# Performance work log

Measured on AMD Instinct MI355X. Metric: run time of the kernel, lower is better.

The kernel has to match this reference:

```python
import jax, jax.numpy as jnp
import numpy as np
from jax.scipy.special import erfc

# ---- model constants (mirroring NeuroNN.__init__ defaults) ----
NEURON_NUM = 6000
RATIO = 0.8
NE = int(NEURON_NUM * RATIO)   # excitatory count (pref ordering: E first)
NI = NEURON_NUM - NE           # inhibitory count (connection blocks: first NI rows/cols)
SCALING_G = 1.0
W_FF = 30.0
SIG_EXT = 5.0
TAU = 1.0
TAU_REF = 1.0
T_INV = 1.0
VT, VR = 20.0, 10.0            # LIF threshold / reset (mV) used inside Ricciardi Phi
DT = 0.1
NMAX = 80                      # Euler2fixedpt total steps (fixed for jit)
NAVG = 30                      # convergence-averaging window
XTOL = 1e-5
XMIN = 1.0

# 64-pt Gauss-Legendre quadrature for the Ricciardi integral
_qn, _qw = np.polynomial.legendre.leggauss(64)
QN = jnp.asarray(_qn, jnp.float32)
QW = jnp.asarray(_qw, jnp.float32)
SQRT_PI = float(np.sqrt(np.pi))


def erfcx(y):
    """Scaled complementary error function exp(y^2)*erfc(y), fp32-safe."""
    y = jnp.clip(y, -9.0, 25.0)  # exp(81) still finite in fp32
    a = jnp.abs(y)
    a_s = jnp.minimum(a, 5.0)
    small = jnp.exp(a_s * a_s) * erfc(a_s)
    a_l = jnp.maximum(a, 5.0)
    large = (1.0 / (SQRT_PI * a_l)) * (1.0 - 0.5 / (a_l * a_l))
    f = jnp.where(a <= 5.0, small, large)
    return jnp.where(y >= 0.0, f, 2.0 * jnp.exp(y * y) - f)


def circ_gauss(x_deg, w):
    # circular gaussian with period 180 deg, same form as the z-row kernel
    return jnp.exp((jnp.cos(x_deg * jnp.pi / 90.0) - 1.0) / (4.0 * (jnp.pi / 180.0 * w) ** 2))


def phi(mu, sigma, tau, tau_ref):
    """Ricciardi LIF transfer: 1/(tau_ref + tau*sqrt(pi)*int_l^u erfcx(-x) dx)."""
    u = (VT - mu) / sigma
    l = (VR - mu) / sigma
    c = 0.5 * (u + l)
    h = 0.5 * (u - l)
    x = c[:, None] + h[:, None] * QN[None, :]          # [N, 64]
    integ = h * jnp.sum(QW[None, :] * erfcx(-x), axis=1)
    return 1.0 / (tau_ref + tau * SQRT_PI * jnp.maximum(integ, 0.0))


def setup_inputs() -> dict:
    key = jax.random.key(0)
    k1, k2, k3 = jax.random.split(key, 3)
    # hyperparameters = [J; P; w], exactly the module's init values
    hyperparameters = jnp.array([[1.99, 1.9, -1.01, -0.79],
                                 [0.11, 0.11, 0.45, 0.45],
                                 [32.0, 32.0, 32.0, 32.0]], dtype=jnp.float32)
    contrast = jax.random.uniform(k1, (1,), jnp.float32)                 # [0,1)
    grating_orientations = jax.random.uniform(k2, (1,), jnp.float32) * 180.0
    # self.pref: E then I linspace over [0,180)
    pref = np.concatenate([np.linspace(0.0, 180.0, NE, endpoint=False),
                           np.linspace(0.0, 180.0, NI, endpoint=False)]).astype(np.float32)
    preferred_orientations = jnp.asarray(pref)
    rand_u = jax.random.uniform(k3, (NEURON_NUM, NEURON_NUM), jnp.float32)
    return {"hyperparameters": hyperparameters, "contrast": contrast,
            "grating_orientations": grating_orientations,
            "preferred_orientations": preferred_orientations, "rand_u": rand_u}


def reference(hyperparameters, contrast, grating_orientations, preferred_orientations, rand_u):
    N = NEURON_NUM
    eff_p, prob_p, width_p = hyperparameters[0], hyperparameters[1], hyperparameters[2]
    i = jnp.arange(N)
    ri = (i < NI).astype(jnp.int32)                      # row block (1 if row < NI)
    conn = ri[:, None] + 2 * ri[None, :]                 # 0/1/2/3 block ids [N,N]
    # circulant roll: np.roll(z_row, i)[j] = z_row[(j-i) % N]
    idx = (i[None, :] - i[:, None]) % N                  # [N,N]
    conn_rolled = ri[:, None] + 2 * (idx < NI).astype(jnp.int32)
    thetas = jnp.linspace(0.0, jnp.pi - 0.01, N)
    cos_term = (jnp.cos(2.0 * thetas) - 1.0)[idx]        # gathered, rolled per row
    width_r = width_p[conn_rolled]
    Z = jnp.exp(cos_term / (4.0 * (jnp.pi / 180.0 * width_r) ** 2))
    # W[i,j] = J * sigmoid(32*(P * z_roll - U))
    W = eff_p[conn] * jax.nn.sigmoid(32.0 * (prob_p[conn] * Z - rand_u))
    W2 = W * W
    # stimulus -> feedforward input
    input_mean = contrast * 20.0 * SCALING_G * circ_gauss(
        grating_orientations - preferred_orientations, W_FF)          # [N]
    input_sd = SIG_EXT

    def step(r, _):
        mu = TAU * (W @ r) + input_mean
        sig = jnp.sqrt(TAU * (W2 @ r) + input_sd ** 2)
        dx = T_INV * (phi(mu, sig, TAU, TAU_REF) - r) * DT
        r2 = r + dx
        conv = jnp.max(jnp.abs(dx) / jnp.maximum(XMIN, jnp.abs(r2))) < XTOL
        return r2, conv

    r0 = jnp.zeros(N, jnp.float32)
    r_fp, convs = jax.lax.scan(step, r0, None, length=NMAX)
    avg_step = jnp.mean(convs[-NAVG:].astype(jnp.float32))
    return r_fp, avg_step
```

## Files before the change

kernel.cpp:

```cpp
#include <hip/hip_runtime.h>
#include <hip/hip_fp16.h>
#include <math.h>

#define NN    6000
#define NPAD  6144
#define NIB   1200
#define NMAXI 80
#define NAVGI 30
#define NBLK  250
#define NTHR  512

#define SQRT_PI_F 1.7724538509055160273f

typedef _Float16 half2_t __attribute__((ext_vector_type(2)));
typedef unsigned uvec8  __attribute__((ext_vector_type(8)));

__device__ __forceinline__ float erfcx_inl(float y) {
  y = fminf(fmaxf(y, -9.0f), 25.0f);
  const float a   = fabsf(y);
  const float a_s = fminf(a, 5.0f);
  const float t   = 1.0f / (1.0f + 0.5f * a_s);
  const float p   = -1.26551223f + t * (1.00002368f + t * (0.37409196f +
                    t * (0.09678418f + t * (-0.18628806f + t * (0.27886807f +
                    t * (-1.13520398f + t * (1.48851587f + t * (-0.82215223f +
                    t * 0.17087277f))))))));
  const float fsm = t * __expf(p);
  const float a_l = fmaxf(a, 5.0f);
  const float flg = (1.0f / (SQRT_PI_F * a_l)) * (1.0f - 0.5f / (a_l * a_l));
  const float f   = (a <= 5.0f) ? fsm : flg;
  return (y >= 0.0f) ? f : 2.0f * __expf(y * y) - f;
}

__device__ __forceinline__ float dot2acc(unsigned w, unsigned r, float acc) {
#if defined(__has_builtin) && __has_builtin(__builtin_amdgcn_fdot2)
  return __builtin_amdgcn_fdot2(__builtin_bit_cast(half2_t, w),
                                __builtin_bit_cast(half2_t, r), acc, false);
#else
  half2_t wh = __builtin_bit_cast(half2_t, w);
  half2_t rh = __builtin_bit_cast(half2_t, r);
  return acc + (float)wh.x * (float)rh.x + (float)wh.y * (float)rh.y;
#endif
}

__device__ __forceinline__ unsigned pksq(unsigned w) {
  half2_t wh = __builtin_bit_cast(half2_t, w);
  half2_t s  = wh * wh;
  return __builtin_bit_cast(unsigned, s);
}

__device__ __forceinline__ void gbar(unsigned* cnt, unsigned* gen, int tid) {
  __syncthreads();
  if (tid == 0) {
    __builtin_amdgcn_fence(__ATOMIC_RELEASE, "agent");
    const unsigned g = __hip_atomic_load(gen, __ATOMIC_RELAXED,
                                         __HIP_MEMORY_SCOPE_AGENT);
    const unsigned old = __hip_atomic_fetch_add(cnt, 1u, __ATOMIC_RELAXED,
                                                __HIP_MEMORY_SCOPE_AGENT);
    if (old == NBLK - 1) {
      __hip_atomic_store(cnt, 0u, __ATOMIC_RELAXED, __HIP_MEMORY_SCOPE_AGENT);
      __hip_atomic_store(gen, g + 1u, __ATOMIC_RELEASE,
                         __HIP_MEMORY_SCOPE_AGENT);
    } else {
      while (__hip_atomic_load(gen, __ATOMIC_RELAXED,
                               __HIP_MEMORY_SCOPE_AGENT) == g)
        __builtin_amdgcn_s_sleep(2);
    }
    __builtin_amdgcn_fence(__ATOMIC_ACQUIRE, "agent");
  }
  __syncthreads();
}

__global__ __launch_bounds__(256) void init_kernel(
    const float* __restrict__ contrast, const float* __restrict__ grat,
    const float* __restrict__ pref, float* __restrict__ g0,
    float* __restrict__ g1, float* __restrict__ meanv,
    float* __restrict__ ctab, float* __restrict__ qn, float* __restrict__ qw,
    unsigned* __restrict__ conv, unsigned* __restrict__ bar)
{
  int t = blockIdx.x * 256 + threadIdx.x;
  if (t < NPAD) { g0[t] = 0.0f; g1[t] = 0.0f; }
  if (t < NN) {
    double th = (3.141592653589793 - 0.01) * (double)t / 5999.0;
    ctab[t] = cosf(2.0f * (float)th) - 1.0f;
    float d  = grat[0] - pref[t];
    float cg = (cosf(d * 3.14159265358979323846f / 90.0f) - 1.0f) / 1.0966227112321508f;
    meanv[t] = contrast[0] * 20.0f * expf(cg);
  }
  if (t < NMAXI) conv[t] = 0u;
  if (t < 2)     bar[t]  = 0u;
  if (blockIdx.x == 0 && threadIdx.x < 64) {
    int m = threadIdx.x;
    double x = cos(3.141592653589793 * (m + 0.75) / 64.5);
    double p0, p1, dp = 1.0;
    for (int it = 0; it < 60; ++it) {
      p0 = 1.0; p1 = x;
      for (int k = 2; k <= 64; ++k) {
        double p2 = ((2.0 * k - 1.0) * x * p1 - (k - 1.0) * p0) / (double)k;
        p0 = p1; p1 = p2;
      }
      dp = 64.0 * (x * p1 - p0) / (x * x - 1.0);
      double step = p1 / dp;
      x -= step;
      if (fabs(step) < 1e-15) break;
    }
    p0 = 1.0; p1 = x;
    for (int k = 2; k <= 64; ++k) {
      double p2 = ((2.0 * k - 1.0) * x * p1 - (k - 1.0) * p0) / (double)k;
      p0 = p1; p1 = p2;
    }
    dp = 64.0 * (x * p1 - p0) / (x * x - 1.0);
    double wgt = 2.0 / ((1.0 - x * x) * dp * dp);
    qn[63 - m] = (float)x;
    qw[63 - m] = (float)wgt;
  }
}

#define GENV(WV, ROW, V, EI, EE, PI, PE, DI, DE, UROW)                        \
  do {                                                                        \
    _Pragma("unroll")                                                         \
    for (int c_ = 0; c_ < 4; ++c_) {                                          \
      const int k_  = (V) * 4 + c_;                                           \
      const int j0_ = k_ * 256 + (lane << 2);                                 \
      float w_[4] = {0.0f, 0.0f, 0.0f, 0.0f};                                 \
      if (j0_ + 3 < NN) {                                                     \
        const float4 uv_ = *reinterpret_cast<const float4*>((UROW) + j0_);    \
        const float us_[4] = {uv_.x, uv_.y, uv_.z, uv_.w};                    \
        _Pragma("unroll")                                                     \
        for (int q_ = 0; q_ < 4; ++q_) {                                      \
          const int j_ = j0_ + q_;                                            \
          int idx_ = j_ - (ROW); idx_ += (idx_ < 0) ? NN : 0;                 \
          const float ct_   = ctabs[idx_];                                    \
          const float eff_  = (j_   < NIB) ? (EI) : (EE);                     \
          const float prob_ = (j_   < NIB) ? (PI) : (PE);                     \
          const float den_  = (idx_ < NIB) ? (DI) : (DE);                     \
          const float Z_  = __expf(ct_ / den_);                               \
          const float tt_ = 32.0f * (prob_ * Z_ - us_[q_]);                   \
          w_[q_] = eff_ / (1.0f + __expf(-tt_));                              \
        }                                                                     \
      }                                                                       \
      half2_t h01_; h01_.x = (_Float16)w_[0]; h01_.y = (_Float16)w_[1];       \
      half2_t h23_; h23_.x = (_Float16)w_[2]; h23_.y = (_Float16)w_[3];       \
      WV[2 * c_]     = __builtin_bit_cast(unsigned, h01_);                    \
      WV[2 * c_ + 1] = __builtin_bit_cast(unsigned, h23_);                    \
    }                                                                         \
  } while (0)

#define ACC3(WAV, WBV, WCV, V)                                                \
  do {                                                                        \
    _Pragma("unroll")                                                         \
    for (int c_ = 0; c_ < 4; ++c_) {                                          \
      const uint2 rr_ = rh2[((V) * 4 + c_) * 64 + lane];                      \
      muA  = dot2acc(WAV[2 * c_],       rr_.x, muA);                          \
      muA  = dot2acc(WAV[2 * c_ + 1],   rr_.y, muA);                          \
      varA = dot2acc(pksq(WAV[2 * c_]),     rr_.x, varA);                     \
      varA = dot2acc(pksq(WAV[2 * c_ + 1]), rr_.y, varA);                     \
      muB  = dot2acc(WBV[2 * c_],       rr_.x, muB);                          \
      muB  = dot2acc(WBV[2 * c_ + 1],   rr_.y, muB);                          \
      varB = dot2acc(pksq(WBV[2 * c_]),     rr_.x, varB);                     \
      varB = dot2acc(pksq(WBV[2 * c_ + 1]), rr_.y, varB);                     \
      muC  = dot2acc(WCV[2 * c_],       rr_.x, muC);                          \
      muC  = dot2acc(WCV[2 * c_ + 1],   rr_.y, muC);                          \
      varC = dot2acc(pksq(WCV[2 * c_]),     rr_.x, varC);                     \
      varC = dot2acc(pksq(WCV[2 * c_ + 1]), rr_.y, varC);                     \
    }                                                                         \
  } while (0)

__global__
__attribute__((amdgpu_flat_work_group_size(NTHR, NTHR)))
__attribute__((amdgpu_waves_per_eu(2, 2))) void solve_kernel(
    const float* __restrict__ hyper, const float* __restrict__ randu,
    const float* __restrict__ ctab, const float* __restrict__ meanv,
    const float* __restrict__ qn, const float* __restrict__ qw,
    float* __restrict__ g0, float* __restrict__ g1,
    float* __restrict__ blkmax, unsigned* __restrict__ bar,
    float* __restrict__ out)
{
  const int tid  = threadIdx.x;
  const int lane = tid & 63;
  const int wv   = tid >> 6;
  const int rowA = blockIdx.x * 24 + wv * 3;
  const int rowB = rowA + 1;
  const int rowC = rowA + 2;

  __shared__ float ctabs[NN];
  __shared__ uint2 rh2[NPAD / 4];
  __shared__ float wmax[8];
  __shared__ float sflag[NAVGI];

  {
    const float4* c4 = reinterpret_cast<const float4*>(ctab);
    float4* l4 = reinterpret_cast<float4*>(ctabs);
    for (int i = tid; i < NN / 4; i += NTHR) l4[i] = c4[i];
  }
  __syncthreads();

  const float qnl = qn[lane];
  const float qwl = qw[lane];
  const float meanA = meanv[rowA];
  const float meanB = meanv[rowB];
  const float meanC = meanv[rowC];

  uvec8 wa0, wa1, wa2, wa3, wa4, wa5;
  uvec8 wb0, wb1, wb2, wb3, wb4, wb5;
  uvec8 wc0, wc1, wc2, wc3, wc4, wc5;
  {
    const float cdg = 0.017453292519943295f;
    {
      const int   ri = (rowA < NIB) ? 1 : 0;
      const float eI = hyper[2 + ri], eE = hyper[0 + ri];
      const float pI = hyper[6 + ri], pE = hyper[4 + ri];
      const float wI = cdg * hyper[10 + ri], wE = cdg * hyper[8 + ri];
      const float dI = 4.0f * (wI * wI), dE = 4.0f * (wE * wE);
      const float* ur = randu + (size_t)rowA * NN;
      GENV(wa0, rowA, 0, eI, eE, pI, pE, dI, dE, ur);
      GENV(wa1, rowA, 1, eI, eE, pI, pE, dI, dE, ur);
      GENV(wa2, rowA, 2, eI, eE, pI, pE, dI, dE, ur);
      GENV(wa3, rowA, 3, eI, eE, pI, pE, dI, dE, ur);
      GENV(wa4, rowA, 4, eI, eE, pI, pE, dI, dE, ur);
      GENV(wa5, rowA, 5, eI, eE, pI, pE, dI, dE, ur);
    }
    {
      const int   ri = (rowB < NIB) ? 1 : 0;
      const float eI = hyper[2 + ri], eE = hyper[0 + ri];
      const float pI = hyper[6 + ri], pE = hyper[4 + ri];
      const float wI = cdg * hyper[10 + ri], wE = cdg * hyper[8 + ri];
      const float dI = 4.0f * (wI * wI), dE = 4.0f * (wE * wE);
      const float* ur = randu + (size_t)rowB * NN;
      GENV(wb0, rowB, 0, eI, eE, pI, pE, dI, dE, ur);
      GENV(wb1, rowB, 1, eI, eE, pI, pE, dI, dE, ur);
      GENV(wb2, rowB, 2, eI, eE, pI, pE, dI, dE, ur);
      GENV(wb3, rowB, 3, eI, eE, pI, pE, dI, dE, ur);
      GENV(wb4, rowB, 4, eI, eE, pI, pE, dI, dE, ur);
      GENV(wb5, rowB, 5, eI, eE, pI, pE, dI, dE, ur);
    }
    {
      const int   ri = (rowC < NIB) ? 1 : 0;
      const float eI = hyper[2 + ri], eE = hyper[0 + ri];
      const float pI = hyper[6 + ri], pE = hyper[4 + ri];
      const float wI = cdg * hyper[10 + ri], wE = cdg * hyper[8 + ri];
      const float dI = 4.0f * (wI * wI), dE = 4.0f * (wE * wE);
      const float* ur = randu + (size_t)rowC * NN;
      GENV(wc0, rowC, 0, eI, eE, pI, pE, dI, dE, ur);
      GENV(wc1, rowC, 1, eI, eE, pI, pE, dI, dE, ur);
      GENV(wc2, rowC, 2, eI, eE, pI, pE, dI, dE, ur);
      GENV(wc3, rowC, 3, eI, eE, pI, pE, dI, dE, ur);
      GENV(wc4, rowC, 4, eI, eE, pI, pE, dI, dE, ur);
      GENV(wc5, rowC, 5, eI, eE, pI, pE, dI, dE, ur);
    }
  }

#pragma unroll 1
  for (int t = 0; t < NMAXI; ++t) {
    const float* rcur = (t & 1) ? g1 : g0;
    float*       rnxt = (t & 1) ? g0 : g1;

    {
      const float4* rc4 = reinterpret_cast<const float4*>(rcur);
#pragma unroll
      for (int s = 0; s < 3; ++s) {
        const float4 s0 = rc4[tid + s * NTHR];
        half2_t a, b;
        a.x = (_Float16)s0.x; a.y = (_Float16)s0.y;
        b.x = (_Float16)s0.z; b.y = (_Float16)s0.w;
        uint2 p;
        p.x = __builtin_bit_cast(unsigned, a);
        p.y = __builtin_bit_cast(unsigned, b);
        rh2[tid + s * NTHR] = p;
      }
    }
    __syncthreads();

    float muA = 0.0f, varA = 0.0f, muB = 0.0f, varB = 0.0f;
    float muC = 0.0f, varC = 0.0f;
    ACC3(wa0, wb0, wc0, 0);
    ACC3(wa1, wb1, wc1, 1);
    ACC3(wa2, wb2, wc2, 2);
    ACC3(wa3, wb3, wc3, 3);
    ACC3(wa4, wb4, wc4, 4);
    ACC3(wa5, wb5, wc5, 5);
#pragma unroll
    for (int off = 32; off > 0; off >>= 1) {
      muA  += __shfl_xor(muA, off);
      varA += __shfl_xor(varA, off);
      muB  += __shfl_xor(muB, off);
      varB += __shfl_xor(varB, off);
      muC  += __shfl_xor(muC, off);
      varC += __shfl_xor(varC, off);
    }

    float ratioM = 0.0f;
#pragma unroll
    for (int rr = 0; rr < 3; ++rr) {
      const int   row = (rr == 0) ? rowA : (rr == 1) ? rowB : rowC;
      float mu  = ((rr == 0) ? muA  : (rr == 1) ? muB  : muC)
                + ((rr == 0) ? meanA : (rr == 1) ? meanB : meanC);
      float var = ((rr == 0) ? varA : (rr == 1) ? varB : varC) + 25.0f;
      const float sig = sqrtf(var);
      const float uu = (20.0f - mu) / sig;
      const float ll = (10.0f - mu) / sig;
      const float cc = 0.5f * (uu + ll);
      const float hh = 0.5f * (uu - ll);
      const float x = cc + hh * qnl;
      float term    = qwl * erfcx_inl(-x);
#pragma unroll
      for (int off = 32; off > 0; off >>= 1) term += __shfl_xor(term, off);
      const float integ = hh * term;
      const float phiv  = 1.0f / (1.0f + SQRT_PI_F * fmaxf(integ, 0.0f));

      const float rold = rcur[row];
      const float dx   = (phiv - rold) * 0.1f;
      const float rnew = rold + dx;
      ratioM = fmaxf(ratioM, fabsf(dx) / fmaxf(1.0f, fabsf(rnew)));
      if (lane == 0) {
        if (t == NMAXI - 1) out[row] = rnew;
        else                rnxt[row] = rnew;
      }
    }
    if (lane == 0) wmax[wv] = ratioM;
    __syncthreads();
    if (tid == 0) {
      float m = wmax[0];
#pragma unroll
      for (int q = 1; q < 8; ++q) m = fmaxf(m, wmax[q]);
      blkmax[(size_t)t * NBLK + blockIdx.x] = m;
    }
    gbar(bar, bar + 1, tid);
  }

  if (blockIdx.x == 0) {
#pragma unroll
    for (int s = 0; s < 4; ++s) {
      const int t = 50 + wv + 8 * s;
      if (t < NMAXI) {
        float m = 0.0f;
        for (int p = lane; p < NBLK; p += 64)
          m = fmaxf(m, blkmax[(size_t)t * NBLK + p]);
#pragma unroll
        for (int off = 32; off > 0; off >>= 1)
          m = fmaxf(m, __shfl_xor(m, off));
        if (lane == 0) sflag[t - 50] = (m < 1e-5f) ? 1.0f : 0.0f;
      }
    }
    __syncthreads();
    if (tid == 0) {
      float s = 0.0f;
#pragma unroll
      for (int q = 0; q < NAVGI; ++q) s += sflag[q];
      out[NN] = s / 30.0f;
    }
  }
}

__global__ __launch_bounds__(256) void genw_kernel(
    const float* __restrict__ hyper, const float* __restrict__ randu,
    const float* __restrict__ ctab, float* __restrict__ Wf)
{
  const int i  = blockIdx.x;
  const int ri = (i < NIB) ? 1 : 0;
  const float eA = hyper[0 + ri], eB = hyper[2 + ri];
  const float pA = hyper[4 + ri], pB = hyper[6 + ri];
  const float c  = 0.017453292519943295f;
  const float wA = c * hyper[8 + ri], wB = c * hyper[10 + ri];
  const float dA = 4.0f * (wA * wA), dB = 4.0f * (wB * wB);
  const float* urow = randu + (size_t)i * NN;
  for (int j4 = threadIdx.x * 4; j4 < NN; j4 += 1024) {
    float4 uv = *reinterpret_cast<const float4*>(urow + j4);
    float us[4] = {uv.x, uv.y, uv.z, uv.w};
    float res[4];
#pragma unroll
    for (int q = 0; q < 4; ++q) {
      int j   = j4 + q;
      int idx = j - i; idx += (idx < 0) ? NN : 0;
      float ct   = ctab[idx];
      float eff  = (j   < NIB) ? eB : eA;
      float prob = (j   < NIB) ? pB : pA;
      float den  = (idx < NIB) ? dB : dA;
      float Z  = __expf(ct / den);
      float tt = 32.0f * (prob * Z - us[q]);
      res[q] = eff / (1.0f + __expf(-tt));
    }
    *reinterpret_cast<float4*>(Wf + (size_t)i * NN + j4) =
        make_float4(res[0], res[1], res[2], res[3]);
  }
}

__global__ __launch_bounds__(256) void iter_kernel(
    const float* __restrict__ Wf, const float* __restrict__ rin,
    float* __restrict__ rout, const float* __restrict__ meanv,
    const float* __restrict__ qn, const float* __restrict__ qw,
    unsigned* __restrict__ convslot)
{
  const int row  = blockIdx.x;
  const int tid  = threadIdx.x;
  const int lane = tid & 63;
  const int wvid = tid >> 6;
  __shared__ float smu[4], svar[4];
  float mu = 0.0f, var = 0.0f;
  const float* wrow = Wf + (size_t)row * NN;
  float4 w[6], r4[6]; bool have[6];
#pragma unroll
  for (int k = 0; k < 6; ++k) {
    const int j = (tid << 2) + (k << 10);
    have[k] = (j < NN);
    if (have[k]) {
      w[k]  = *reinterpret_cast<const float4*>(wrow + j);
      r4[k] = *reinterpret_cast<const float4*>(rin + j);
    }
  }
#pragma unroll
  for (int k = 0; k < 6; ++k) if (have[k]) {
    mu  += w[k].x * r4[k].x + w[k].y * r4[k].y + w[k].z * r4[k].z + w[k].w * r4[k].w;
    var += w[k].x * w[k].x * r4[k].x + w[k].y * w[k].y * r4[k].y
         + w[k].z * w[k].z * r4[k].z + w[k].w * w[k].w * r4[k].w;
  }
#pragma unroll
  for (int off = 32; off > 0; off >>= 1) {
    mu  += __shfl_xor(mu, off);
    var += __shfl_xor(var, off);
  }
  if (lane == 0) { smu[wvid] = mu; svar[wvid] = var; }
  __syncthreads();
  if (tid < 64) {
    mu  = smu[0] + smu[1] + smu[2] + smu[3];
    var = svar[0] + svar[1] + svar[2] + svar[3];
    mu += meanv[row]; var += 25.0f;
    const float sig = sqrtf(var);
    const float uu = (20.0f - mu) / sig;
    const float ll = (10.0f - mu) / sig;
    const float cc = 0.5f * (uu + ll);
    const float hh = 0.5f * (uu - ll);
    const float x = cc + hh * qn[lane];
    float term    = qw[lane] * erfcx_inl(-x);
#pragma unroll
    for (int off = 32; off > 0; off >>= 1) term += __shfl_xor(term, off);
    const float integ = hh * term;
    const float phiv  = 1.0f / (1.0f + SQRT_PI_F * fmaxf(integ, 0.0f));
    const float rold = rin[row];
    const float dx   = (phiv - rold) * 0.1f;
    const float rnew = rold + dx;
    if (lane == 0) {
      rout[row] = rnew;
      const float ratio = fabsf(dx) / fmaxf(1.0f, fabsf(rnew));
      atomicMax(convslot, __float_as_uint(ratio));
    }
  }
}

__global__ __launch_bounds__(256) void final_kernel(
    const float* __restrict__ rfin, const unsigned* __restrict__ conv,
    float* __restrict__ out)
{
  int t = blockIdx.x * 256 + threadIdx.x;
  if (t < NN) out[t] = rfin[t];
  if (t == 6000) {
    float s = 0.0f;
    for (int k = NMAXI - NAVGI; k < NMAXI; ++k)
      s += (__uint_as_float(conv[k]) < 1e-5f) ? 1.0f : 0.0f;
    out[NN] = s / 30.0f;
  }
}

extern "C" void kernel_launch(void* const* d_in, const int* in_sizes, int n_in,
                              void* d_out, int out_size, void* d_ws, size_t ws_size,
                              hipStream_t stream) {
  const float* hyper    = (const float*)d_in[0];
  const float* contrast = (const float*)d_in[1];
  const float* grat     = (const float*)d_in[2];
  const float* pref     = (const float*)d_in[3];
  const float* randu    = (const float*)d_in[4];
  float* out = (float*)d_out;

  char* ws = (char*)d_ws;
  float*    g0     = (float*)(ws + 0);
  float*    g1     = (float*)(ws + 24576);
  float*    mn     = (float*)(ws + 49152);
  float*    ctab   = (float*)(ws + 73152);
  float*    qn     = (float*)(ws + 97152);
  float*    qw     = (float*)(ws + 97408);
  unsigned* conv   = (unsigned*)(ws + 97664);
  unsigned* bar    = (unsigned*)(ws + 97984);
  float*    blkmax = (float*)(ws + 98304);
  float*    Wf     = (float*)(ws + 262144);

  init_kernel<<<24, 256, 0, stream>>>(contrast, grat, pref, g0, g1, mn, ctab,
                                      qn, qw, conv, bar);

  {
    const float* a_hyper = hyper;  const float* a_randu = randu;
    const float* a_ctab  = ctab;   const float* a_mn    = mn;
    const float* a_qn    = qn;     const float* a_qw    = qw;
    float* a_g0 = g0; float* a_g1 = g1; float* a_bm = blkmax;
    unsigned* a_bar = bar; float* a_out = out;
    void* args[11] = {&a_hyper, &a_randu, &a_ctab, &a_mn, &a_qn, &a_qw,
                      &a_g0, &a_g1, &a_bm, &a_bar, &a_out};
    hipError_t err = hipLaunchCooperativeKernel(
        (const void*)solve_kernel, dim3(NBLK), dim3(NTHR), args, 0, stream);
    if (err == hipSuccess) return;
  }

  genw_kernel<<<NN, 256, 0, stream>>>(hyper, randu, ctab, Wf);
  float* rb[2] = {g0, g1};
  for (int t = 0; t < NMAXI; ++t) {
    const float* rin = rb[t & 1];
    float*       rou = rb[(t + 1) & 1];
    iter_kernel<<<NN, 256, 0, stream>>>(Wf, rin, rou, mn, qn, qw, conv + t);
  }
  final_kernel<<<24, 256, 0, stream>>>(rb[0], conv, out);
}
```

Measured before the change: 1.665 ms.

## Stream fp16 weights from global memory instead of holding them in registers

The fp16 weight rows are no longer kept resident in registers for all 80 iterations. They are written once to a global workspace buffer and re-read each iteration with 16-byte vector loads, using 8 elements per lane and a uint4 shared r-vector. This frees the very large register footprint so the waves_per_eu constraint can be dropped. In exchange, every iteration re-reads about 72 MB of weights from L2/HBM, which risks making the loop bandwidth-bound.

```diff
diff --git a/kernel.cpp b/kernel.cpp
--- a/kernel.cpp
+++ b/kernel.cpp
@@ -13,7 +13,6 @@
 #define SQRT_PI_F 1.7724538509055160273f
 
 typedef _Float16 half2_t __attribute__((ext_vector_type(2)));
-typedef unsigned uvec8  __attribute__((ext_vector_type(8)));
 
 __device__ __forceinline__ float erfcx_inl(float y) {
   y = fminf(fmaxf(y, -9.0f), 25.0f);
@@ -115,63 +114,12 @@
   }
 }
 
-#define GENV(WV, ROW, V, EI, EE, PI, PE, DI, DE, UROW)                        \
-  do {                                                                        \
-    _Pragma("unroll")                                                         \
-    for (int c_ = 0; c_ < 4; ++c_) {                                          \
-      const int k_  = (V) * 4 + c_;                                           \
-      const int j0_ = k_ * 256 + (lane << 2);                                 \
-      float w_[4] = {0.0f, 0.0f, 0.0f, 0.0f};                                 \
-      if (j0_ + 3 < NN) {                                                     \
-        const float4 uv_ = *reinterpret_cast<const float4*>((UROW) + j0_);    \
-        const float us_[4] = {uv_.x, uv_.y, uv_.z, uv_.w};                    \
-        _Pragma("unroll")                                                     \
-        for (int q_ = 0; q_ < 4; ++q_) {                                      \
-          const int j_ = j0_ + q_;                                            \
-          int idx_ = j_ - (ROW); idx_ += (idx_ < 0) ? NN : 0;                 \
-          const float ct_   = ctabs[idx_];                                    \
-          const float eff_  = (j_   < NIB) ? (EI) : (EE);                     \
-          const float prob_ = (j_   < NIB) ? (PI) : (PE);                     \
-          const float den_  = (idx_ < NIB) ? (DI) : (DE);                     \
-          const float Z_  = __expf(ct_ / den_);                               \
-          const float tt_ = 32.0f * (prob_ * Z_ - us_[q_]);                   \
-          w_[q_] = eff_ / (1.0f + __expf(-tt_));                              \
-        }                                                                     \
-      }                                                                       \
-      half2_t h01_; h01_.x = (_Float16)w_[0]; h01_.y = (_Float16)w_[1];       \
-      half2_t h23_; h23_.x = (_Float16)w_[2]; h23_.y = (_Float16)w_[3];       \
-      WV[2 * c_]     = __builtin_bit_cast(unsigned, h01_);                    \
-      WV[2 * c_ + 1] = __builtin_bit_cast(unsigned, h23_);                    \
-    }                                                                         \
-  } while (0)
-
-#define ACC3(WAV, WBV, WCV, V)                                                \
-  do {                                                                        \
-    _Pragma("unroll")                                                         \
-    for (int c_ = 0; c_ < 4; ++c_) {                                          \
-      const uint2 rr_ = rh2[((V) * 4 + c_) * 64 + lane];                      \
-      muA  = dot2acc(WAV[2 * c_],       rr_.x, muA);                          \
-      muA  = dot2acc(WAV[2 * c_ + 1],   rr_.y, muA);                          \
-      varA = dot2acc(pksq(WAV[2 * c_]),     rr_.x, varA);                     \
-      varA = dot2acc(pksq(WAV[2 * c_ + 1]), rr_.y, varA);                     \
-      muB  = dot2acc(WBV[2 * c_],       rr_.x, muB);                          \
-      muB  = dot2acc(WBV[2 * c_ + 1],   rr_.y, muB);                          \
-      varB = dot2acc(pksq(WBV[2 * c_]),     rr_.x, varB);                     \
-      varB = dot2acc(pksq(WBV[2 * c_ + 1]), rr_.y, varB);                     \
-      muC  = dot2acc(WCV[2 * c_],       rr_.x, muC);                          \
-      muC  = dot2acc(WCV[2 * c_ + 1],   rr_.y, muC);                          \
-      varC = dot2acc(pksq(WCV[2 * c_]),     rr_.x, varC);                     \
-      varC = dot2acc(pksq(WCV[2 * c_ + 1]), rr_.y, varC);                     \
-    }                                                                         \
-  } while (0)
-
-__global__
-__attribute__((amdgpu_flat_work_group_size(NTHR, NTHR)))
-__attribute__((amdgpu_waves_per_eu(2, 2))) void solve_kernel(
+__global__ __launch_bounds__(NTHR) void solve_kernel(
     const float* __restrict__ hyper, const float* __restrict__ randu,
     const float* __restrict__ ctab, const float* __restrict__ meanv,
     const float* __restrict__ qn, const float* __restrict__ qw,
     float* __restrict__ g0, float* __restrict__ g1,
+    unsigned short* __restrict__ Wp,
     float* __restrict__ blkmax, unsigned* __restrict__ bar,
     float* __restrict__ out)
 {
@@ -179,11 +127,9 @@
   const int lane = tid & 63;
   const int wv   = tid >> 6;
   const int rowA = blockIdx.x * 24 + wv * 3;
-  const int rowB = rowA + 1;
-  const int rowC = rowA + 2;
 
   __shared__ float ctabs[NN];
-  __shared__ uint2 rh2[NPAD / 4];
+  __shared__ uint4 rh4[NPAD / 8];
   __shared__ float wmax[8];
   __shared__ float sflag[NAVGI];
 
@@ -197,57 +143,63 @@
   const float qnl = qn[lane];
   const float qwl = qw[lane];
   const float meanA = meanv[rowA];
-  const float meanB = meanv[rowB];
-  const float meanC = meanv[rowC];
-
-  uvec8 wa0, wa1, wa2, wa3, wa4, wa5;
-  uvec8 wb0, wb1, wb2, wb3, wb4, wb5;
-  uvec8 wc0, wc1, wc2, wc3, wc4, wc5;
+  const float meanB = meanv[rowA + 1];
+  const float meanC = meanv[rowA + 2];
+
   {
     const float cdg = 0.017453292519943295f;
-    {
-      const int   ri = (rowA < NIB) ? 1 : 0;
+    for (int rr = 0; rr < 3; ++rr) {
+      const int row = rowA + rr;
+      const int ri  = (row < NIB) ? 1 : 0;
       const float eI = hyper[2 + ri], eE = hyper[0 + ri];
       const float pI = hyper[6 + ri], pE = hyper[4 + ri];
       const float wI = cdg * hyper[10 + ri], wE = cdg * hyper[8 + ri];
       const float dI = 4.0f * (wI * wI), dE = 4.0f * (wE * wE);
-      const float* ur = randu + (size_t)rowA * NN;
-      GENV(wa0, rowA, 0, eI, eE, pI, pE, dI, dE, ur);
-      GENV(wa1, rowA, 1, eI, eE, pI, pE, dI, dE, ur);
-      GENV(wa2, rowA, 2, eI, eE, pI, pE, dI, dE, ur);
-      GENV(wa3, rowA, 3, eI, eE, pI, pE, dI, dE, ur);
-      GENV(wa4, rowA, 4, eI, eE, pI, pE, dI, dE, ur);
-      GENV(wa5, rowA, 5, eI, eE, pI, pE, dI, dE, ur);
-    }
-    {
-      const int   ri = (rowB < NIB) ? 1 : 0;
-      const float eI = hyper[2 + ri], eE = hyper[0 + ri];
-      const float pI = hyper[6 + ri], pE = hyper[4 + ri];
-      const float wI = cdg * hyper[10 + ri], wE = cdg * hyper[8 + ri];
-      const float dI = 4.0f * (wI * wI), dE = 4.0f * (wE * wE);
-      const float* ur = randu + (size_t)rowB * NN;
-      GENV(wb0, rowB, 0, eI, eE, pI, pE, dI, dE, ur);
-      GENV(wb1, rowB, 1, eI, eE, pI, pE, dI, dE, ur);
-      GENV(wb2, rowB, 2, eI, eE, pI, pE, dI, dE, ur);
-      GENV(wb3, rowB, 3, eI, eE, pI, pE, dI, dE, ur);
-      GENV(wb4, rowB, 4, eI, eE, pI, pE, dI, dE, ur);
-      GENV(wb5, rowB, 5, eI, eE, pI, pE, dI, dE, ur);
-    }
-    {
-      const int   ri = (rowC < NIB) ? 1 : 0;
-      const float eI = hyper[2 + ri], eE = hyper[0 + ri];
-      const float pI = hyper[6 + ri], pE = hyper[4 + ri];
-      const float wI = cdg * hyper[10 + ri], wE = cdg * hyper[8 + ri];
-      const float dI = 4.0f * (wI * wI), dE = 4.0f * (wE * wE);
-      const float* ur = randu + (size_t)rowC * NN;
-      GENV(wc0, rowC, 0, eI, eE, pI, pE, dI, dE, ur);
-      GENV(wc1, rowC, 1, eI, eE, pI, pE, dI, dE, ur);
-      GENV(wc2, rowC, 2, eI, eE, pI, pE, dI, dE, ur);
-      GENV(wc3, rowC, 3, eI, eE, pI, pE, dI, dE, ur);
-      GENV(wc4, rowC, 4, eI, eE, pI, pE, dI, dE, ur);
-      GENV(wc5, rowC, 5, eI, eE, pI, pE, dI, dE, ur);
-    }
-  }
+      const float* ur = randu + (size_t)row * NN;
+      unsigned short* wrow = Wp + (size_t)row * NPAD;
+#pragma unroll
+      for (int k = 0; k < 12; ++k) {
+        const int j0 = k * 512 + lane * 8;
+        float w[8];
+        if (j0 < NN) {
+          const float4 u0 = *reinterpret_cast<const float4*>(ur + j0);
+          const float4 u1 = *reinterpret_cast<const float4*>(ur + j0 + 4);
+          const float us[8] = {u0.x, u0.y, u0.z, u0.w, u1.x, u1.y, u1.z, u1.w};
+#pragma unroll
+          for (int q = 0; q < 8; ++q) {
+            const int j = j0 + q;
+            int idx = j - row; idx += (idx < 0) ? NN : 0;
+            const float ct   = ctabs[idx];
+            const float eff  = (j   < NIB) ? eI : eE;
+            const float prob = (j   < NIB) ? pI : pE;
+            const float den  = (idx < NIB) ? dI : dE;
+            const float Z  = __expf(ct / den);
+            const float tt = 32.0f * (prob * Z - us[q]);
+            w[q] = eff / (1.0f + __expf(-tt));
+          }
+        } else {
+#pragma unroll
+          for (int q = 0; q < 8; ++q) w[q] = 0.0f;
+        }
+        uint4 pk;
+        half2_t h;
+        h.x = (_Float16)w[0]; h.y = (_Float16)w[1];
+        pk.x = __builtin_bit_cast(unsigned, h);
+        h.x = (_Float16)w[2]; h.y = (_Float16)w[3];
+        pk.y = __builtin_bit_cast(unsigned, h);
+        h.x = (_Float16)w[4]; h.y = (_Float16)w[5];
+        pk.z = __builtin_bit_cast(unsigned, h);
+        h.x = (_Float16)w[6]; h.y = (_Float16)w[7];
+        pk.w = __builtin_bit_cast(unsigned, h);
+        *reinterpret_cast<uint4*>(wrow + j0) = pk;
+      }
+    }
+  }
+  __syncthreads();
+
+  const unsigned short* wrA = Wp + (size_t)rowA * NPAD;
+  const unsigned short* wrB = Wp + (size_t)(rowA + 1) * NPAD;
+  const unsigned short* wrC = Wp + (size_t)(rowA + 2) * NPAD;
 
 #pragma unroll 1
   for (int t = 0; t < NMAXI; ++t) {
@@ -256,28 +208,46 @@
 
     {
       const float4* rc4 = reinterpret_cast<const float4*>(rcur);
-#pragma unroll
-      for (int s = 0; s < 3; ++s) {
-        const float4 s0 = rc4[tid + s * NTHR];
-        half2_t a, b;
-        a.x = (_Float16)s0.x; a.y = (_Float16)s0.y;
-        b.x = (_Float16)s0.z; b.y = (_Float16)s0.w;
-        uint2 p;
-        p.x = __builtin_bit_cast(unsigned, a);
-        p.y = __builtin_bit_cast(unsigned, b);
-        rh2[tid + s * NTHR] = p;
+      for (int i = tid; i < NPAD / 8; i += NTHR) {
+        const float4 lo = rc4[i * 2];
+        const float4 hi = rc4[i * 2 + 1];
+        uint4 pk;
+        half2_t h;
+        h.x = (_Float16)lo.x; h.y = (_Float16)lo.y;
+        pk.x = __builtin_bit_cast(unsigned, h);
+        h.x = (_Float16)lo.z; h.y = (_Float16)lo.w;
+        pk.y = __builtin_bit_cast(unsigned, h);
+        h.x = (_Float16)hi.x; h.y = (_Float16)hi.y;
+        pk.z = __builtin_bit_cast(unsigned, h);
+        h.x = (_Float16)hi.z; h.y = (_Float16)hi.w;
+        pk.w = __builtin_bit_cast(unsigned, h);
+        rh4[i] = pk;
       }
     }
     __syncthreads();
 
     float muA = 0.0f, varA = 0.0f, muB = 0.0f, varB = 0.0f;
     float muC = 0.0f, varC = 0.0f;
-    ACC3(wa0, wb0, wc0, 0);
-    ACC3(wa1, wb1, wc1, 1);
-    ACC3(wa2, wb2, wc2, 2);
-    ACC3(wa3, wb3, wc3, 3);
-    ACC3(wa4, wb4, wc4, 4);
-    ACC3(wa5, wb5, wc5, 5);
+#pragma unroll
+    for (int k = 0; k < 12; ++k) {
+      const int off = k * 512 + lane * 8;
+      const uint4 a = *reinterpret_cast<const uint4*>(wrA + off);
+      const uint4 b = *reinterpret_cast<const uint4*>(wrB + off);
+      const uint4 c = *reinterpret_cast<const uint4*>(wrC + off);
+      const uint4 rr = rh4[k * 64 + lane];
+      muA  = dot2acc(a.x, rr.x, muA);  muA  = dot2acc(a.y, rr.y, muA);
+      muA  = dot2acc(a.z, rr.z, muA);  muA  = dot2acc(a.w, rr.w, muA);
+      varA = dot2acc(pksq(a.x), rr.x, varA); varA = dot2acc(pksq(a.y), rr.y, varA);
+      varA = dot2acc(pksq(a.z), rr.z, varA); varA = dot2acc(pksq(a.w), rr.w, varA);
+      muB  = dot2acc(b.x, rr.x, muB);  muB  = dot2acc(b.y, rr.y, muB);
+      muB  = dot2acc(b.z, rr.z, muB);  muB  = dot2acc(b.w, rr.w, muB);
+      varB = dot2acc(pksq(b.x), rr.x, varB); varB = dot2acc(pksq(b.y), rr.y, varB);
+      varB = dot2acc(pksq(b.z), rr.z, varB); varB = dot2acc(pksq(b.w), rr.w, varB);
+      muC  = dot2acc(c.x, rr.x, muC);  muC  = dot2acc(c.y, rr.y, muC);
+      muC  = dot2acc(c.z, rr.z, muC);  muC  = dot2acc(c.w, rr.w, muC);
+      varC = dot2acc(pksq(c.x), rr.x, varC); varC = dot2acc(pksq(c.y), rr.y, varC);
+      varC = dot2acc(pksq(c.z), rr.z, varC); varC = dot2acc(pksq(c.w), rr.w, varC);
+    }
 #pragma unroll
     for (int off = 32; off > 0; off >>= 1) {
       muA  += __shfl_xor(muA, off);
@@ -291,7 +261,7 @@
     float ratioM = 0.0f;
 #pragma unroll
     for (int rr = 0; rr < 3; ++rr) {
-      const int   row = (rr == 0) ? rowA : (rr == 1) ? rowB : rowC;
+      const int   row = rowA + rr;
       float mu  = ((rr == 0) ? muA  : (rr == 1) ? muB  : muC)
                 + ((rr == 0) ? meanA : (rr == 1) ? meanB : meanC);
       float var = ((rr == 0) ? varA : (rr == 1) ? varB : varC) + 25.0f;
@@ -480,6 +450,7 @@
   unsigned* conv   = (unsigned*)(ws + 97664);
   unsigned* bar    = (unsigned*)(ws + 97984);
   float*    blkmax = (float*)(ws + 98304);
+  unsigned short* Wp = (unsigned short*)(ws + 262144);
   float*    Wf     = (float*)(ws + 262144);
 
   init_kernel<<<24, 256, 0, stream>>>(contrast, grat, pref, g0, g1, mn, ctab,
@@ -489,10 +460,11 @@
     const float* a_hyper = hyper;  const float* a_randu = randu;
     const float* a_ctab  = ctab;   const float* a_mn    = mn;
     const float* a_qn    = qn;     const float* a_qw    = qw;
-    float* a_g0 = g0; float* a_g1 = g1; float* a_bm = blkmax;
-    unsigned* a_bar = bar; float* a_out = out;
-    void* args[11] = {&a_hyper, &a_randu, &a_ctab, &a_mn, &a_qn, &a_qw,
-                      &a_g0, &a_g1, &a_bm, &a_bar, &a_out};
+    float* a_g0 = g0; float* a_g1 = g1;
+    unsigned short* a_wp = Wp;
+    float* a_bm = blkmax; unsigned* a_bar = bar; float* a_out = out;
+    void* args[12] = {&a_hyper, &a_randu, &a_ctab, &a_mn, &a_qn, &a_qw,
+                      &a_g0, &a_g1, &a_wp, &a_bm, &a_bar, &a_out};
     hipError_t err = hipLaunchCooperativeKernel(
         (const void*)solve_kernel, dim3(NBLK), dim3(NTHR), args, 0, stream);
     if (err == hipSuccess) return;
```

Result: slower. 2.296 ms (+38.0%).
